# Optimization experiments

Measured on AMD Instinct MI355X. Metric: run time of the kernel, lower is better.

The kernel has to match this reference:

```python
import jax, jax.numpy as jnp
import numpy as np

B, S, HID = 2, 2048, 1024
H, D = 16, 64  # num query heads, head_dim; single shared KV head
SCALE = D ** -0.5


def setup_inputs() -> dict:
    key = jax.random.key(0)
    k1, k2, k3, k4, k5 = jax.random.split(key, 5)
    return {
        "hidden_states": jax.random.normal(k1, (B, S, HID), dtype=jnp.float32),
        "Wq": jax.random.normal(k2, (HID, HID), dtype=jnp.float32) * 0.02,
        "Wk": jax.random.normal(k3, (HID, D), dtype=jnp.float32) * 0.02,
        "Wv": jax.random.normal(k4, (HID, D), dtype=jnp.float32) * 0.02,
        "Wo": jax.random.normal(k5, (HID, HID), dtype=jnp.float32) * 0.02,
    }


def reference(hidden_states, Wq, Wk, Wv, Wo):
    b, s, _ = hidden_states.shape
    # projections: Q has H heads; K/V have a single shared head of dim D
    q = (hidden_states @ Wq).reshape(b, s, H, D)  # [B,S,H,D]
    k = hidden_states @ Wk                        # [B,S,D]
    v = hidden_states @ Wv                        # [B,S,D]
    # scores: broadcast single KV head across all query heads
    scores = jnp.einsum("bqhd,bkd->bhqk", q, k) * SCALE  # [B,H,S,S]
    attn = jax.nn.softmax(scores, axis=-1)
    out = jnp.einsum("bhqk,bkd->bqhd", attn, v).reshape(b, s, HID)
    return out @ Wo
```

## Files before the change

### kernel.cpp

```cpp
#include <hip/hip_runtime.h>
#include <math.h>

#define BATCH 2
#define SEQ   2048
#define HID   1024
#define NH    16
#define HD    64
#define MTOT  (BATCH * SEQ)

#define PST 72
#define VST 136
#define WTS 69

#define EXP_C1 0.1803368801111255f

typedef __attribute__((ext_vector_type(8))) short short8;
typedef __attribute__((ext_vector_type(4))) float floatx4;
typedef __attribute__((ext_vector_type(16))) float floatx16;
typedef __attribute__((ext_vector_type(4))) unsigned int uint4v;

#define MFMA32(a, b, c) __builtin_amdgcn_mfma_f32_32x32x16_bf16(a, b, c, 0, 0, 0)
#define MFMA16(a, b, c) __builtin_amdgcn_mfma_f32_16x16x32_bf16(a, b, c, 0, 0, 0)

static __device__ __forceinline__ floatx16 zero16() {
    floatx16 z;
    #pragma unroll
    for (int i = 0; i < 16; ++i) z[i] = 0.f;
    return z;
}

__device__ __forceinline__ unsigned short f2bf(float x) {
    unsigned u = __float_as_uint(x);
    u += 0x7FFF + ((u >> 16) & 1);
    return (unsigned short)(u >> 16);
}
__device__ __forceinline__ float bf2f(unsigned short h) {
    return __uint_as_float((unsigned)h << 16);
}

__device__ __forceinline__ void gld16(const unsigned short* g, unsigned short* l) {
    __builtin_amdgcn_global_load_lds(
        (const __attribute__((address_space(1))) unsigned int*)g,
        (__attribute__((address_space(3))) unsigned int*)l, 16, 0, 0);
}


__global__ __launch_bounds__(256)
void presplit_kernel(const float* __restrict__ Wq, const float* __restrict__ Wk,
                     const float* __restrict__ Wv, const float* __restrict__ Wo,
                     const float* __restrict__ X,
                     unsigned short* __restrict__ WqTh,
                     unsigned short* __restrict__ WkTh,
                     unsigned short* __restrict__ WvTh,
                     unsigned short* __restrict__ WoTh, unsigned short* __restrict__ WoTl,
                     unsigned short* __restrict__ Xh)
{
    __shared__ __align__(16) float Wtmp[64][WTS];
    const int tid = threadIdx.x;
    int bx = blockIdx.x;

    if (bx >= 544) {
        size_t i0 = (size_t)(bx - 544) * 4096 + tid * 16;
        float f[16];
        *(float4*)&f[0]  = *(const float4*)(X + i0 + 0);
        *(float4*)&f[4]  = *(const float4*)(X + i0 + 4);
        *(float4*)&f[8]  = *(const float4*)(X + i0 + 8);
        *(float4*)&f[12] = *(const float4*)(X + i0 + 12);
        unsigned short hh[16];
        #pragma unroll
        for (int e = 0; e < 16; ++e) hh[e] = f2bf(f[e]);
        const int m  = (bx - 544) * 4 + (tid >> 6);
        const int k0 = (tid & 63) * 16;
        const int m32 = m >> 5, mi = (m >> 4) & 1, tr = m & 15;
        #pragma unroll
        for (int c = 0; c < 2; ++c) {
            const int k = k0 + c * 8;
            const int ktx = k >> 6, ksx = (k >> 5) & 1, qd = (k >> 3) & 3;
            size_t off = (((size_t)(m32 * 16 + ktx) * 2 + ksx) * 2 + mi) * 512
                       + (qd * 16 + tr) * 8;
            *(uint4*)(Xh + off) = *(uint4*)&hh[c * 8];
        }
        return;
    }

    const float* W; unsigned short *Th, *Tl; int ldw, kt, nt;
    if (bx < 256)      { W = Wq; Th = WqTh; Tl = nullptr; ldw = HID; kt = bx >> 4; nt = bx & 15; }
    else if (bx < 272) { W = Wk; Th = WkTh; Tl = nullptr; ldw = HD;  kt = bx - 256; nt = 0; }
    else if (bx < 288) { W = Wv; Th = WvTh; Tl = nullptr; ldw = HD;  kt = bx - 272; nt = 0; }
    else               { W = Wo; Th = WoTh; Tl = WoTl;   ldw = HID; bx -= 288; kt = bx >> 4; nt = bx & 15; }
    const int k0 = kt * 64, n0 = nt * 64;

    {
        const int wk = tid >> 2, wn = (tid & 3) * 16;
        const float* wp = W + (size_t)(k0 + wk) * ldw + n0 + wn;
        float f[16];
        *(float4*)&f[0]  = *(const float4*)(wp + 0);
        *(float4*)&f[4]  = *(const float4*)(wp + 4);
        *(float4*)&f[8]  = *(const float4*)(wp + 8);
        *(float4*)&f[12] = *(const float4*)(wp + 12);
        #pragma unroll
        for (int e = 0; e < 16; ++e) Wtmp[wk][wn + e] = f[e];
    }
    __syncthreads();
    {
        const int rn = tid >> 2, rk = (tid & 3) * 16;
        float f[16];
        #pragma unroll
        for (int e = 0; e < 16; ++e) f[e] = Wtmp[rk + e][rn];
        unsigned short hh[16];
        #pragma unroll
        for (int e = 0; e < 16; ++e) hh[e] = f2bf(f[e]);
        const int sub = rn >> 4, tw = rn & 15;
        const size_t tb = ((size_t)nt * 16 + kt) * 4096;
        const int ksA = rk >> 5,       qA = (rk >> 3) & 3;
        const int ksB = (rk + 8) >> 5, qB = ((rk + 8) >> 3) & 3;
        const size_t offA = tb + (size_t)(ksA * 4 + sub) * 512 + (qA * 16 + tw) * 8;
        const size_t offB = tb + (size_t)(ksB * 4 + sub) * 512 + (qB * 16 + tw) * 8;
        *(uint4*)(Th + offA) = *(uint4*)&hh[0];
        *(uint4*)(Th + offB) = *(uint4*)&hh[8];
        if (Tl) {
            unsigned short ll[16];
            #pragma unroll
            for (int e = 0; e < 16; ++e) ll[e] = f2bf(f[e] - bf2f(hh[e]));
            *(uint4*)(Tl + offA) = *(uint4*)&ll[0];
            *(uint4*)(Tl + offB) = *(uint4*)&ll[8];
        }
    }
}

__global__ __launch_bounds__(512)
void qkv_kernel(const unsigned short* __restrict__ Xfo,
                const unsigned short* __restrict__ WqTh,
                const unsigned short* __restrict__ WkTh,
                const unsigned short* __restrict__ WvTh,
                unsigned short* __restrict__ Qh,
                unsigned short* __restrict__ Kh, unsigned short* __restrict__ Vth)
{
    __shared__ __align__(16) unsigned short Wst[2][4096];

    const int tid  = threadIdx.x;
    const int wave = tid >> 6, lane = tid & 63;
    const int t = lane & 15, quad = lane >> 4;
    const int m0 = blockIdx.x * 128;
    const int nb = blockIdx.y;

    const unsigned short *WTh; int nt;
    if (nb < 16)       { WTh = WqTh; nt = nb; }
    else if (nb == 16) { WTh = WkTh; nt = 0; }
    else               { WTh = WvTh; nt = 0; }

    floatx4 acc[4];
    #pragma unroll
    for (int sub = 0; sub < 4; ++sub) acc[sub] = (floatx4){0.f,0.f,0.f,0.f};

    const int m32 = blockIdx.x * 4 + (wave >> 1), mi = wave & 1;
    const size_t abase = ((size_t)m32 * 16) * 2048 + (size_t)mi * 512 + lane * 8;

    auto STAGE = [&](int buf, int kt) {
        const size_t tb = ((size_t)nt * 16 + kt) * 4096 + wave * 512 + lane * 8;
        gld16(WTh + tb, &Wst[buf][wave * 512]);
    };
    auto COMPUTE = [&](int buf, short8 a0, short8 a1) {
        #pragma unroll
        for (int ksq = 0; ksq < 2; ++ksq) {
            short8 am = ksq ? a1 : a0;
            #pragma unroll
            for (int sub = 0; sub < 4; ++sub) {
                short8 bh = *(const short8*)&Wst[buf][(ksq * 4 + sub) * 512 + lane * 8];
                acc[sub] = MFMA16(am, bh, acc[sub]);
            }
        }
    };

    short8 a0 = *(const short8*)(Xfo + abase);
    short8 a1 = *(const short8*)(Xfo + abase + 1024);
    STAGE(0, 0);
    __syncthreads();

    int cur = 0;
    for (int kt = 0; kt < HID / 64 - 1; ++kt) {
        STAGE(cur ^ 1, kt + 1);
        short8 n0 = *(const short8*)(Xfo + abase + (size_t)(kt + 1) * 2048);
        short8 n1 = *(const short8*)(Xfo + abase + (size_t)(kt + 1) * 2048 + 1024);

        COMPUTE(cur, a0, a1);

        __syncthreads();
        a0 = n0; a1 = n1;
        cur ^= 1;
    }
    COMPUTE(cur, a0, a1);

    #pragma unroll
    for (int sub = 0; sub < 4; ++sub)
        #pragma unroll
        for (int r = 0; r < 4; ++r) {
            int g = m0 + wave * 16 + quad * 4 + r;
            int d = sub * 16 + t;
            if (nb < 16) {
                int b = g >> 11, s = g & (SEQ - 1);
                Qh[((size_t)(b * NH + nb) * SEQ + s) * HD + d] =
                    f2bf(acc[sub][r] * EXP_C1);
            } else if (nb == 16) {
                Kh[(size_t)g * HD + d] = f2bf(acc[sub][r]);
            } else {
                int b = g >> 11, s = g & (SEQ - 1);
                Vth[(size_t)b * HD * SEQ + (size_t)d * SEQ + s] = f2bf(acc[sub][r]);
            }
        }
}

__global__ __launch_bounds__(512, 4)
void flash_kernel(const unsigned short* __restrict__ Qhg,
                  const unsigned short* __restrict__ Khg,
                  const unsigned short* __restrict__ Vthg,
                  unsigned short* __restrict__ Oh)
{
    __shared__ __align__(16) char smem[35840];
    unsigned short (*Ksh)[PST] = (unsigned short (*)[PST])smem;
    unsigned short (*Vsh)[VST] = (unsigned short (*)[VST])(smem + 18432);

    const int tid  = threadIdx.x;
    const int wave = tid >> 6, lane = tid & 63;
    const int lq = lane & 31, hi = lane >> 5;
    const int qw = wave >> 1;
    const int ks = wave & 1;
    const int klq = (lq & ~12) | ((lq & 4) << 1) | ((lq & 8) >> 1);

    const int q0 = blockIdx.x * 128;
    const int h  = blockIdx.y;
    const int b  = blockIdx.z;

    short8 qreg[4];
    {
        const unsigned short* qp =
            Qhg + ((size_t)(b * NH + h) * SEQ + q0 + qw * 32 + lq) * HD + hi * 8;
        #pragma unroll
        for (int dc = 0; dc < 4; ++dc) qreg[dc] = *(const short8*)(qp + dc * 16);
    }

    const unsigned short* Kh_b  = Khg  + (size_t)b * SEQ * HD;
    const unsigned short* Vth_b = Vthg + (size_t)b * HD * SEQ;

    const int krA = tid >> 3,          kcA = (tid & 7) * 8;
    const int krB = 64 + (tid >> 3),   kcB = kcA;
    const int vrA = tid >> 4,          vcA = (tid & 15) * 8;
    const int vrB = 32 + (tid >> 4),   vcB = vcA;

    floatx16 o0 = zero16(), o1 = zero16(), ol = zero16();
    short8 onesB;
    #pragma unroll
    for (int j = 0; j < 8; ++j) onesB[j] = (short)0x3F80;

    uint4 gk0 = *(const uint4*)(Kh_b + (size_t)krA * HD + kcA);
    uint4 gk1 = *(const uint4*)(Kh_b + (size_t)krB * HD + kcB);
    uint4 gv0 = *(const uint4*)(Vth_b + (size_t)vrA * SEQ + vcA);
    uint4 gv1 = *(const uint4*)(Vth_b + (size_t)vrB * SEQ + vcB);

    for (int kt = 0; kt < SEQ / 128; ++kt) {
        __syncthreads();
        *(uint4*)&Ksh[krA][kcA] = gk0;
        *(uint4*)&Ksh[krB][kcB] = gk1;
        *(uint4*)&Vsh[vrA][vcA] = gv0;
        *(uint4*)&Vsh[vrB][vcB] = gv1;
        if (kt + 1 < SEQ / 128) {
            gk0 = *(const uint4*)(Kh_b + (size_t)((kt + 1) * 128 + krA) * HD + kcA);
            gk1 = *(const uint4*)(Kh_b + (size_t)((kt + 1) * 128 + krB) * HD + kcB);
            gv0 = *(const uint4*)(Vth_b + (size_t)vrA * SEQ + (kt + 1) * 128 + vcA);
            gv1 = *(const uint4*)(Vth_b + (size_t)vrB * SEQ + (kt + 1) * 128 + vcB);
        }
        __syncthreads();

        #pragma unroll
        for (int c = 0; c < 2; ++c) {
            const int kb = ks * 64 + c * 32;

            floatx16 sf = zero16();
            __builtin_amdgcn_s_setprio(1);
            #pragma unroll
            for (int dc = 0; dc < 4; ++dc) {
                short8 kf = *(const short8*)&Ksh[kb + klq][dc * 16 + hi * 8];
                sf = MFMA32(kf, qreg[dc], sf);
            }
            __builtin_amdgcn_s_setprio(0);

            #pragma unroll
            for (int mm = 0; mm < 2; ++mm) {
                unsigned uu[8];
                #pragma unroll
                for (int j = 0; j < 8; ++j)
                    uu[j] = __float_as_uint(exp2f(sf[mm * 8 + j]));
                uint4v pw;
                pw.x = (uu[0] >> 16) | (uu[1] & 0xFFFF0000u);
                pw.y = (uu[2] >> 16) | (uu[3] & 0xFFFF0000u);
                pw.z = (uu[4] >> 16) | (uu[5] & 0xFFFF0000u);
                pw.w = (uu[6] >> 16) | (uu[7] & 0xFFFF0000u);
                short8 pa = __builtin_bit_cast(short8, pw);
                short8 v0 = *(const short8*)&Vsh[lq][kb + mm * 16 + hi * 8];
                short8 v1 = *(const short8*)&Vsh[32 + lq][kb + mm * 16 + hi * 8];
                __builtin_amdgcn_s_setprio(1);
                ol = MFMA32(pa, onesB, ol);
                o0 = MFMA32(pa, v0, o0);
                o1 = MFMA32(pa, v1, o1);
                __builtin_amdgcn_s_setprio(0);
            }
        }
    }

    __syncthreads();
    float* cb  = (float*)smem;
    float* cbl = (float*)(smem + 33792);
    const int cbase = (qw * 64 + lane) * 33;
    if (ks) {
        #pragma unroll
        for (int r = 0; r < 16; ++r) { cb[cbase + r] = o0[r]; cb[cbase + 16 + r] = o1[r]; }
        if (lq == 0) {
            #pragma unroll
            for (int r = 0; r < 16; ++r) cbl[(qw * 2 + hi) * 16 + r] = ol[r];
        }
    }
    __syncthreads();
    if (!ks) {
        const int m32 = b * 64 + blockIdx.x * 4 + qw;
        #pragma unroll
        for (int r = 0; r < 16; ++r) {
            int qr = (r & 3) + 8 * (r >> 2) + 4 * hi;
            float ltot = ol[r] + cbl[(qw * 2 + hi) * 16 + r];
            float inv = 1.0f / ltot;
            float a0 = o0[r] + cb[cbase + r];
            float a1 = o1[r] + cb[cbase + 16 + r];
            int mi = qr >> 4, tr = qr & 15;
            size_t base = (((size_t)(m32 * 16 + h) * 2 + 0) * 2 + mi) * 512
                        + ((lq >> 3) * 16 + tr) * 8 + (lq & 7);
            Oh[base]        = f2bf(a0 * inv);
            Oh[base + 1024] = f2bf(a1 * inv);
        }
    }
}

__global__ __launch_bounds__(512)
void out_proj_kernel(const unsigned short* __restrict__ Ofo,
                     const unsigned short* __restrict__ WoTh,
                     const unsigned short* __restrict__ WoTl,
                     float* __restrict__ out)
{
    __shared__ __align__(16) unsigned short Wst[2][2][4096];

    const int tid  = threadIdx.x;
    const int wave = tid >> 6, lane = tid & 63;
    const int t = lane & 15, quad = lane >> 4;
    const int m0 = blockIdx.x * 128;
    const int nt = blockIdx.y;

    floatx4 acc[4];
    #pragma unroll
    for (int sub = 0; sub < 4; ++sub) acc[sub] = (floatx4){0.f,0.f,0.f,0.f};

    const int m32 = blockIdx.x * 4 + (wave >> 1), mi = wave & 1;
    const size_t abase = ((size_t)m32 * 16) * 2048 + (size_t)mi * 512 + lane * 8;

    auto STAGE = [&](int buf, int kt) {
        const size_t tb = ((size_t)nt * 16 + kt) * 4096 + wave * 512 + lane * 8;
        gld16(WoTh + tb, &Wst[buf][0][wave * 512]);
        gld16(WoTl + tb, &Wst[buf][1][wave * 512]);
    };
    auto COMPUTE = [&](int buf, short8 a0, short8 a1) {
        #pragma unroll
        for (int ksq = 0; ksq < 2; ++ksq) {
            short8 am = ksq ? a1 : a0;
            #pragma unroll
            for (int sub = 0; sub < 4; ++sub) {
                short8 bh = *(const short8*)&Wst[buf][0][(ksq * 4 + sub) * 512 + lane * 8];
                short8 bl = *(const short8*)&Wst[buf][1][(ksq * 4 + sub) * 512 + lane * 8];
                acc[sub] = MFMA16(am, bh, acc[sub]);
                acc[sub] = MFMA16(am, bl, acc[sub]);
            }
        }
    };

    short8 a0 = *(const short8*)(Ofo + abase);
    short8 a1 = *(const short8*)(Ofo + abase + 1024);
    STAGE(0, 0);
    __syncthreads();

    int cur = 0;
    for (int kt = 0; kt < HID / 64 - 1; ++kt) {
        STAGE(cur ^ 1, kt + 1);
        short8 n0 = *(const short8*)(Ofo + abase + (size_t)(kt + 1) * 2048);
        short8 n1 = *(const short8*)(Ofo + abase + (size_t)(kt + 1) * 2048 + 1024);

        COMPUTE(cur, a0, a1);

        __syncthreads();
        a0 = n0; a1 = n1;
        cur ^= 1;
    }
    COMPUTE(cur, a0, a1);

    const int n0 = nt * 64;
    #pragma unroll
    for (int sub = 0; sub < 4; ++sub)
        #pragma unroll
        for (int r = 0; r < 4; ++r)
            out[(size_t)(m0 + wave * 16 + quad * 4 + r) * HID
                + n0 + sub * 16 + t] = acc[sub][r];
}

extern "C" void kernel_launch(void* const* d_in, const int* in_sizes, int n_in,
                              void* d_out, int out_size, void* d_ws, size_t ws_size,
                              hipStream_t stream)
{
    const float* X  = (const float*)d_in[0];
    const float* Wq = (const float*)d_in[1];
    const float* Wk = (const float*)d_in[2];
    const float* Wv = (const float*)d_in[3];
    const float* Wo = (const float*)d_in[4];
    float* out = (float*)d_out;

    unsigned short* Qh = (unsigned short*)d_out;
    unsigned short* Xh = Qh + (size_t)BATCH * NH * SEQ * HD;

    char* ws = (char*)d_ws;
    const size_t SZ_WQ = (size_t)HID * HID * 2;
    const size_t SZ_WK = (size_t)HD * HID * 2;
    unsigned short* WqTh = (unsigned short*)(ws);
    unsigned short* WkTh = (unsigned short*)(ws + 2*SZ_WQ);
    unsigned short* WvTh = (unsigned short*)(ws + 2*SZ_WQ + 2*SZ_WK);
    unsigned short* WoTh = (unsigned short*)(ws + 2*SZ_WQ + 4*SZ_WK);
    unsigned short* WoTl = (unsigned short*)(ws + 3*SZ_WQ + 4*SZ_WK);
    unsigned short* Kh   = (unsigned short*)(ws + 4*SZ_WQ + 4*SZ_WK);
    unsigned short* Vth  = (unsigned short*)(ws + 4*SZ_WQ + 4*SZ_WK + (size_t)MTOT*HD*2);
    unsigned short* Oh   = (unsigned short*)(ws + 4*SZ_WQ + 4*SZ_WK + (size_t)MTOT*HD*4);

    presplit_kernel<<<dim3(1568), 256, 0, stream>>>(Wq, Wk, Wv, Wo, X,
        WqTh, WkTh, WvTh, WoTh, WoTl, Xh);
    qkv_kernel<<<dim3(MTOT / 128, 18), 512, 0, stream>>>(Xh,
        WqTh, WkTh, WvTh, Qh, Kh, Vth);
    flash_kernel<<<dim3(SEQ / 128, NH, BATCH), 512, 0, stream>>>(Qh, Kh, Vth, Oh);
    out_proj_kernel<<<dim3(MTOT / 128, HID / 64), 512, 0, stream>>>(Oh, WoTh, WoTl, out);
}
```

Before: 174.4 us.

## Double-buffer K/V tiles in flash kernel with one barrier per iteration

Changes the flash attention kernel to keep two K/V tiles in dynamically sized LDS. The next tile is written into the alternate buffer while the current one is consumed, and the global prefetch for tile kt+2 is issued between the two P·V halves. Both score MFMA chains are computed up front so the two 32-key chunks get more instruction-level parallelism. This removes one of the two barriers per iteration, but doubles LDS use to about 70KB per block, which may lower occupancy from the requested 4 blocks per CU, and it holds more live registers.

```diff
diff --git a/kernel.cpp b/kernel.cpp
--- a/kernel.cpp
+++ b/kernel.cpp
@@ -11,6 +11,7 @@
 #define PST 72
 #define VST 136
 #define WTS 69
+#define FBUF 35840
 
 #define EXP_C1 0.1803368801111255f
 
@@ -216,9 +217,7 @@
                   const unsigned short* __restrict__ Vthg,
                   unsigned short* __restrict__ Oh)
 {
-    __shared__ __align__(16) char smem[35840];
-    unsigned short (*Ksh)[PST] = (unsigned short (*)[PST])smem;
-    unsigned short (*Vsh)[VST] = (unsigned short (*)[VST])(smem + 18432);
+    extern __shared__ __align__(16) char smem[];
 
     const int tid  = threadIdx.x;
     const int wave = tid >> 6, lane = tid & 63;
@@ -243,47 +242,62 @@
     const unsigned short* Vth_b = Vthg + (size_t)b * HD * SEQ;
 
     const int krA = tid >> 3,          kcA = (tid & 7) * 8;
-    const int krB = 64 + (tid >> 3),   kcB = kcA;
+    const int krB = 64 + (tid >> 3);
     const int vrA = tid >> 4,          vcA = (tid & 15) * 8;
-    const int vrB = 32 + (tid >> 4),   vcB = vcA;
+    const int vrB = 32 + (tid >> 4);
 
     floatx16 o0 = zero16(), o1 = zero16(), ol = zero16();
     short8 onesB;
     #pragma unroll
     for (int j = 0; j < 8; ++j) onesB[j] = (short)0x3F80;
 
+    const int NT = SEQ / 128;
+
     uint4 gk0 = *(const uint4*)(Kh_b + (size_t)krA * HD + kcA);
-    uint4 gk1 = *(const uint4*)(Kh_b + (size_t)krB * HD + kcB);
+    uint4 gk1 = *(const uint4*)(Kh_b + (size_t)krB * HD + kcA);
     uint4 gv0 = *(const uint4*)(Vth_b + (size_t)vrA * SEQ + vcA);
-    uint4 gv1 = *(const uint4*)(Vth_b + (size_t)vrB * SEQ + vcB);
-
-    for (int kt = 0; kt < SEQ / 128; ++kt) {
-        __syncthreads();
-        *(uint4*)&Ksh[krA][kcA] = gk0;
-        *(uint4*)&Ksh[krB][kcB] = gk1;
-        *(uint4*)&Vsh[vrA][vcA] = gv0;
-        *(uint4*)&Vsh[vrB][vcB] = gv1;
-        if (kt + 1 < SEQ / 128) {
-            gk0 = *(const uint4*)(Kh_b + (size_t)((kt + 1) * 128 + krA) * HD + kcA);
-            gk1 = *(const uint4*)(Kh_b + (size_t)((kt + 1) * 128 + krB) * HD + kcB);
-            gv0 = *(const uint4*)(Vth_b + (size_t)vrA * SEQ + (kt + 1) * 128 + vcA);
-            gv1 = *(const uint4*)(Vth_b + (size_t)vrB * SEQ + (kt + 1) * 128 + vcB);
-        }
-        __syncthreads();
-
-        #pragma unroll
-        for (int c = 0; c < 2; ++c) {
-            const int kb = ks * 64 + c * 32;
-
-            floatx16 sf = zero16();
-            __builtin_amdgcn_s_setprio(1);
-            #pragma unroll
-            for (int dc = 0; dc < 4; ++dc) {
-                short8 kf = *(const short8*)&Ksh[kb + klq][dc * 16 + hi * 8];
-                sf = MFMA32(kf, qreg[dc], sf);
-            }
-            __builtin_amdgcn_s_setprio(0);
-
+    uint4 gv1 = *(const uint4*)(Vth_b + (size_t)vrB * SEQ + vcA);
+    {
+        unsigned short (*K0)[PST] = (unsigned short (*)[PST])smem;
+        unsigned short (*V0)[VST] = (unsigned short (*)[VST])(smem + 18432);
+        *(uint4*)&K0[krA][kcA] = gk0;  *(uint4*)&K0[krB][kcA] = gk1;
+        *(uint4*)&V0[vrA][vcA] = gv0;  *(uint4*)&V0[vrB][vcA] = gv1;
+    }
+    gk0 = *(const uint4*)(Kh_b + (size_t)(128 + krA) * HD + kcA);
+    gk1 = *(const uint4*)(Kh_b + (size_t)(128 + krB) * HD + kcA);
+    gv0 = *(const uint4*)(Vth_b + (size_t)vrA * SEQ + 128 + vcA);
+    gv1 = *(const uint4*)(Vth_b + (size_t)vrB * SEQ + 128 + vcA);
+    __syncthreads();
+
+    for (int kt = 0; kt < NT; ++kt) {
+        char* base = smem + (kt & 1) * FBUF;
+        unsigned short (*Ksh)[PST] = (unsigned short (*)[PST])base;
+        unsigned short (*Vsh)[VST] = (unsigned short (*)[VST])(base + 18432);
+
+        if (kt + 1 < NT) {
+            char* nb = smem + ((kt + 1) & 1) * FBUF;
+            unsigned short (*Kw)[PST] = (unsigned short (*)[PST])nb;
+            unsigned short (*Vw)[VST] = (unsigned short (*)[VST])(nb + 18432);
+            *(uint4*)&Kw[krA][kcA] = gk0;  *(uint4*)&Kw[krB][kcA] = gk1;
+            *(uint4*)&Vw[vrA][vcA] = gv0;  *(uint4*)&Vw[vrB][vcA] = gv1;
+        }
+
+        const int kb0 = ks * 64, kb1 = ks * 64 + 32;
+        floatx16 sfA = zero16(), sfB = zero16();
+        __builtin_amdgcn_s_setprio(1);
+        #pragma unroll
+        for (int dc = 0; dc < 4; ++dc) {
+            short8 kfA = *(const short8*)&Ksh[kb0 + klq][dc * 16 + hi * 8];
+            sfA = MFMA32(kfA, qreg[dc], sfA);
+        }
+        #pragma unroll
+        for (int dc = 0; dc < 4; ++dc) {
+            short8 kfB = *(const short8*)&Ksh[kb1 + klq][dc * 16 + hi * 8];
+            sfB = MFMA32(kfB, qreg[dc], sfB);
+        }
+        __builtin_amdgcn_s_setprio(0);
+
+        auto PROCESS = [&](const floatx16& sf, int kb) {
             #pragma unroll
             for (int mm = 0; mm < 2; ++mm) {
                 unsigned uu[8];
@@ -304,10 +318,19 @@
                 o1 = MFMA32(pa, v1, o1);
                 __builtin_amdgcn_s_setprio(0);
             }
-        }
-    }
-
-    __syncthreads();
+        };
+
+        PROCESS(sfA, kb0);
+        if (kt + 2 < NT) {
+            gk0 = *(const uint4*)(Kh_b + (size_t)((kt + 2) * 128 + krA) * HD + kcA);
+            gk1 = *(const uint4*)(Kh_b + (size_t)((kt + 2) * 128 + krB) * HD + kcA);
+            gv0 = *(const uint4*)(Vth_b + (size_t)vrA * SEQ + (kt + 2) * 128 + vcA);
+            gv1 = *(const uint4*)(Vth_b + (size_t)vrB * SEQ + (kt + 2) * 128 + vcA);
+        }
+        PROCESS(sfB, kb1);
+        __syncthreads();
+    }
+
     float* cb  = (float*)smem;
     float* cbl = (float*)(smem + 33792);
     const int cbase = (qw * 64 + lane) * 33;
@@ -436,6 +459,6 @@
         WqTh, WkTh, WvTh, WoTh, WoTl, Xh);
     qkv_kernel<<<dim3(MTOT / 128, 18), 512, 0, stream>>>(Xh,
         WqTh, WkTh, WvTh, Qh, Kh, Vth);
-    flash_kernel<<<dim3(SEQ / 128, NH, BATCH), 512, 0, stream>>>(Qh, Kh, Vth, Oh);
+    flash_kernel<<<dim3(SEQ / 128, NH, BATCH), 512, 2 * FBUF, stream>>>(Qh, Kh, Vth, Oh);
     out_proj_kernel<<<dim3(MTOT / 128, HID / 64), 512, 0, stream>>>(Oh, WoTh, WoTl, out);
 }
```

Result: faster. 168.0 us (-3.7%).

## Restructure flash attention with tiled swizzled KV layout and async LDS double-buffering

Applied to the files above, without the earlier changes.

The QKV projection now writes Q, K and V in 128-row tiles with XOR swizzling, so the flash kernel can copy whole tiles into LDS with global_load_lds into double buffers and avoid register staging. The flash kernel moves to 1024 threads with a 4-way key split per query group, keeps Q in LDS, and replaces the ones-matrix MFMA row-sum with a scalar partial sum of the bf16-truncated exponentials. The partial results are reduced across four waves through LDS in sequential rounds. This costs 80KB of dynamic LDS per block, which limits occupancy, and adds extra reduction syncs.

```diff
diff --git a/kernel.cpp b/kernel.cpp
--- a/kernel.cpp
+++ b/kernel.cpp
@@ -8,9 +8,10 @@
 #define HD    64
 #define MTOT  (BATCH * SEQ)
 
-#define PST 72
-#define VST 136
 #define WTS 69
+
+#define FSTG 32768
+#define FQOF 65536
 
 #define EXP_C1 0.1803368801111255f
 
@@ -42,6 +43,10 @@
     __builtin_amdgcn_global_load_lds(
         (const __attribute__((address_space(1))) unsigned int*)g,
         (__attribute__((address_space(3))) unsigned int*)l, 16, 0, 0);
+}
+
+__device__ __forceinline__ unsigned packtr(unsigned hi, unsigned lo) {
+    return __builtin_amdgcn_perm(hi, lo, 0x07060302u);
 }
 
 
@@ -133,8 +138,8 @@
                 const unsigned short* __restrict__ WqTh,
                 const unsigned short* __restrict__ WkTh,
                 const unsigned short* __restrict__ WvTh,
-                unsigned short* __restrict__ Qh,
-                unsigned short* __restrict__ Kh, unsigned short* __restrict__ Vth)
+                unsigned short* __restrict__ Qhf,
+                unsigned short* __restrict__ Khf, unsigned short* __restrict__ Vthf)
 {
     __shared__ __align__(16) unsigned short Wst[2][4096];
 
@@ -197,143 +202,139 @@
         for (int r = 0; r < 4; ++r) {
             int g = m0 + wave * 16 + quad * 4 + r;
             int d = sub * 16 + t;
+            int b = g >> 11, sfull = g & (SEQ - 1);
+            int tt = sfull >> 7, sl = sfull & 127;
+            int xor8 = (sl & 7) << 3;
             if (nb < 16) {
-                int b = g >> 11, s = g & (SEQ - 1);
-                Qh[((size_t)(b * NH + nb) * SEQ + s) * HD + d] =
+                Qhf[(((size_t)(b * NH + nb) * 16 + tt) * 8192) + sl * 64 + (d ^ xor8)] =
                     f2bf(acc[sub][r] * EXP_C1);
             } else if (nb == 16) {
-                Kh[(size_t)g * HD + d] = f2bf(acc[sub][r]);
+                Khf[((size_t)b * 16 + tt) * 8192 + sl * 64 + (d ^ xor8)] =
+                    f2bf(acc[sub][r]);
             } else {
-                int b = g >> 11, s = g & (SEQ - 1);
-                Vth[(size_t)b * HD * SEQ + (size_t)d * SEQ + s] = f2bf(acc[sub][r]);
+                Vthf[((size_t)b * 16 + tt) * 8192 + d * 128 + (sl ^ ((d & 7) << 3))] =
+                    f2bf(acc[sub][r]);
             }
         }
 }
 
-__global__ __launch_bounds__(512, 4)
-void flash_kernel(const unsigned short* __restrict__ Qhg,
-                  const unsigned short* __restrict__ Khg,
-                  const unsigned short* __restrict__ Vthg,
+__global__ __launch_bounds__(1024, 8)
+void flash_kernel(const unsigned short* __restrict__ Qhf,
+                  const unsigned short* __restrict__ Khf,
+                  const unsigned short* __restrict__ Vthf,
                   unsigned short* __restrict__ Oh)
 {
-    __shared__ __align__(16) char smem[35840];
-    unsigned short (*Ksh)[PST] = (unsigned short (*)[PST])smem;
-    unsigned short (*Vsh)[VST] = (unsigned short (*)[VST])(smem + 18432);
+    extern __shared__ __align__(16) char smem[];
 
     const int tid  = threadIdx.x;
     const int wave = tid >> 6, lane = tid & 63;
     const int lq = lane & 31, hi = lane >> 5;
-    const int qw = wave >> 1;
-    const int ks = wave & 1;
+    const int qg = wave >> 2;
+    const int kq = wave & 3;
     const int klq = (lq & ~12) | ((lq & 4) << 1) | ((lq & 8) >> 1);
 
-    const int q0 = blockIdx.x * 128;
     const int h  = blockIdx.y;
     const int b  = blockIdx.z;
 
-    short8 qreg[4];
+    const unsigned short* Qt = Qhf + (((size_t)(b * NH + h) * 16 + blockIdx.x) * 8192);
+    const unsigned short* Kb = Khf + ((size_t)b * 16) * 8192;
+    const unsigned short* Vb = Vthf + ((size_t)b * 16) * 8192;
+
+    unsigned short* Qlds = (unsigned short*)(smem + FQOF);
+
+    floatx16 o0 = zero16(), o1 = zero16();
+    float l_part = 0.f;
+
+    const int NT = SEQ / 128;
+
+    gld16(Qt + tid * 8, Qlds + tid * 8);
     {
-        const unsigned short* qp =
-            Qhg + ((size_t)(b * NH + h) * SEQ + q0 + qw * 32 + lq) * HD + hi * 8;
-        #pragma unroll
-        for (int dc = 0; dc < 4; ++dc) qreg[dc] = *(const short8*)(qp + dc * 16);
-    }
-
-    const unsigned short* Kh_b  = Khg  + (size_t)b * SEQ * HD;
-    const unsigned short* Vth_b = Vthg + (size_t)b * HD * SEQ;
-
-    const int krA = tid >> 3,          kcA = (tid & 7) * 8;
-    const int krB = 64 + (tid >> 3),   kcB = kcA;
-    const int vrA = tid >> 4,          vcA = (tid & 15) * 8;
-    const int vrB = 32 + (tid >> 4),   vcB = vcA;
-
-    floatx16 o0 = zero16(), o1 = zero16(), ol = zero16();
-    short8 onesB;
-    #pragma unroll
-    for (int j = 0; j < 8; ++j) onesB[j] = (short)0x3F80;
-
-    uint4 gk0 = *(const uint4*)(Kh_b + (size_t)krA * HD + kcA);
-    uint4 gk1 = *(const uint4*)(Kh_b + (size_t)krB * HD + kcB);
-    uint4 gv0 = *(const uint4*)(Vth_b + (size_t)vrA * SEQ + vcA);
-    uint4 gv1 = *(const uint4*)(Vth_b + (size_t)vrB * SEQ + vcB);
-
-    for (int kt = 0; kt < SEQ / 128; ++kt) {
+        unsigned short* K0 = (unsigned short*)(smem);
+        unsigned short* V0 = (unsigned short*)(smem + 16384);
+        gld16(Kb + tid * 8, K0 + tid * 8);
+        gld16(Vb + tid * 8, V0 + tid * 8);
+    }
+    __syncthreads();
+
+    const int kb = kq * 32;
+    const int qrow = qg * 32 + lq;
+    const int qxor = (lq & 7) << 3;
+    const int vxor = (lq & 7) << 3;
+
+    for (int kt = 0; kt < NT; ++kt) {
+        unsigned short* Kl = (unsigned short*)(smem + (kt & 1) * FSTG);
+        unsigned short* Vl = (unsigned short*)(smem + (kt & 1) * FSTG + 16384);
+
+        if (kt + 1 < NT) {
+            unsigned short* Kn = (unsigned short*)(smem + ((kt + 1) & 1) * FSTG);
+            unsigned short* Vn = (unsigned short*)(smem + ((kt + 1) & 1) * FSTG + 16384);
+            gld16(Kb + (size_t)(kt + 1) * 8192 + tid * 8, Kn + tid * 8);
+            gld16(Vb + (size_t)(kt + 1) * 8192 + tid * 8, Vn + tid * 8);
+        }
+
+        floatx16 sf = zero16();
+        __builtin_amdgcn_s_setprio(1);
+        #pragma unroll
+        for (int dc = 0; dc < 4; ++dc) {
+            const int col = dc * 16 + hi * 8;
+            short8 kf = *(const short8*)&Kl[(kb + klq) * 64 + (col ^ ((klq & 7) << 3))];
+            short8 qf = *(const short8*)&Qlds[qrow * 64 + (col ^ qxor)];
+            sf = MFMA32(kf, qf, sf);
+        }
+        __builtin_amdgcn_s_setprio(0);
+
+        #pragma unroll
+        for (int mm = 0; mm < 2; ++mm) {
+            uint4v pw;
+            #pragma unroll
+            for (int wj = 0; wj < 4; ++wj) {
+                unsigned e0 = __float_as_uint(exp2f(sf[mm * 8 + wj * 2]));
+                unsigned e1 = __float_as_uint(exp2f(sf[mm * 8 + wj * 2 + 1]));
+                l_part += __uint_as_float(e0 & 0xFFFF0000u)
+                        + __uint_as_float(e1 & 0xFFFF0000u);
+                pw[wj] = packtr(e1, e0);
+            }
+            short8 pa = __builtin_bit_cast(short8, pw);
+            const int scol = kb + mm * 16 + hi * 8;
+            short8 v0 = *(const short8*)&Vl[lq * 128 + (scol ^ vxor)];
+            short8 v1 = *(const short8*)&Vl[(32 + lq) * 128 + (scol ^ vxor)];
+            __builtin_amdgcn_s_setprio(1);
+            o0 = MFMA32(pa, v0, o0);
+            o1 = MFMA32(pa, v1, o1);
+            __builtin_amdgcn_s_setprio(0);
+        }
         __syncthreads();
-        *(uint4*)&Ksh[krA][kcA] = gk0;
-        *(uint4*)&Ksh[krB][kcB] = gk1;
-        *(uint4*)&Vsh[vrA][vcA] = gv0;
-        *(uint4*)&Vsh[vrB][vcB] = gv1;
-        if (kt + 1 < SEQ / 128) {
-            gk0 = *(const uint4*)(Kh_b + (size_t)((kt + 1) * 128 + krA) * HD + kcA);
-            gk1 = *(const uint4*)(Kh_b + (size_t)((kt + 1) * 128 + krB) * HD + kcB);
-            gv0 = *(const uint4*)(Vth_b + (size_t)vrA * SEQ + (kt + 1) * 128 + vcA);
-            gv1 = *(const uint4*)(Vth_b + (size_t)vrB * SEQ + (kt + 1) * 128 + vcB);
+    }
+
+    float l_wave = l_part + __shfl_xor(l_part, 32);
+    float* cb = (float*)smem;
+    const int cbase = (qg * 64 + lane) * 33;
+    #pragma unroll
+    for (int rr = 1; rr < 4; ++rr) {
+        if (kq == rr) {
+            #pragma unroll
+            for (int r = 0; r < 16; ++r) { cb[cbase + r] = o0[r]; cb[cbase + 16 + r] = o1[r]; }
+            cb[cbase + 32] = l_wave;
         }
         __syncthreads();
-
-        #pragma unroll
-        for (int c = 0; c < 2; ++c) {
-            const int kb = ks * 64 + c * 32;
-
-            floatx16 sf = zero16();
-            __builtin_amdgcn_s_setprio(1);
-            #pragma unroll
-            for (int dc = 0; dc < 4; ++dc) {
-                short8 kf = *(const short8*)&Ksh[kb + klq][dc * 16 + hi * 8];
-                sf = MFMA32(kf, qreg[dc], sf);
-            }
-            __builtin_amdgcn_s_setprio(0);
-
-            #pragma unroll
-            for (int mm = 0; mm < 2; ++mm) {
-                unsigned uu[8];
-                #pragma unroll
-                for (int j = 0; j < 8; ++j)
-                    uu[j] = __float_as_uint(exp2f(sf[mm * 8 + j]));
-                uint4v pw;
-                pw.x = (uu[0] >> 16) | (uu[1] & 0xFFFF0000u);
-                pw.y = (uu[2] >> 16) | (uu[3] & 0xFFFF0000u);
-                pw.z = (uu[4] >> 16) | (uu[5] & 0xFFFF0000u);
-                pw.w = (uu[6] >> 16) | (uu[7] & 0xFFFF0000u);
-                short8 pa = __builtin_bit_cast(short8, pw);
-                short8 v0 = *(const short8*)&Vsh[lq][kb + mm * 16 + hi * 8];
-                short8 v1 = *(const short8*)&Vsh[32 + lq][kb + mm * 16 + hi * 8];
-                __builtin_amdgcn_s_setprio(1);
-                ol = MFMA32(pa, onesB, ol);
-                o0 = MFMA32(pa, v0, o0);
-                o1 = MFMA32(pa, v1, o1);
-                __builtin_amdgcn_s_setprio(0);
-            }
-        }
-    }
-
-    __syncthreads();
-    float* cb  = (float*)smem;
-    float* cbl = (float*)(smem + 33792);
-    const int cbase = (qw * 64 + lane) * 33;
-    if (ks) {
-        #pragma unroll
-        for (int r = 0; r < 16; ++r) { cb[cbase + r] = o0[r]; cb[cbase + 16 + r] = o1[r]; }
-        if (lq == 0) {
-            #pragma unroll
-            for (int r = 0; r < 16; ++r) cbl[(qw * 2 + hi) * 16 + r] = ol[r];
-        }
-    }
-    __syncthreads();
-    if (!ks) {
-        const int m32 = b * 64 + blockIdx.x * 4 + qw;
+        if (kq == 0) {
+            #pragma unroll
+            for (int r = 0; r < 16; ++r) { o0[r] += cb[cbase + r]; o1[r] += cb[cbase + 16 + r]; }
+            l_wave += cb[cbase + 32];
+        }
+        __syncthreads();
+    }
+    if (kq == 0) {
+        const int m32 = b * 64 + blockIdx.x * 4 + qg;
         #pragma unroll
         for (int r = 0; r < 16; ++r) {
             int qr = (r & 3) + 8 * (r >> 2) + 4 * hi;
-            float ltot = ol[r] + cbl[(qw * 2 + hi) * 16 + r];
-            float inv = 1.0f / ltot;
-            float a0 = o0[r] + cb[cbase + r];
-            float a1 = o1[r] + cb[cbase + 16 + r];
+            float inv = 1.0f / __shfl(l_wave, qr);
             int mi = qr >> 4, tr = qr & 15;
             size_t base = (((size_t)(m32 * 16 + h) * 2 + 0) * 2 + mi) * 512
                         + ((lq >> 3) * 16 + tr) * 8 + (lq & 7);
-            Oh[base]        = f2bf(a0 * inv);
-            Oh[base + 1024] = f2bf(a1 * inv);
+            Oh[base]        = f2bf(o0[r] * inv);
+            Oh[base + 1024] = f2bf(o1[r] * inv);
         }
     }
 }
@@ -417,8 +418,8 @@
     const float* Wo = (const float*)d_in[4];
     float* out = (float*)d_out;
 
-    unsigned short* Qh = (unsigned short*)d_out;
-    unsigned short* Xh = Qh + (size_t)BATCH * NH * SEQ * HD;
+    unsigned short* Qhf = (unsigned short*)d_out;
+    unsigned short* Xh  = Qhf + (size_t)BATCH * NH * SEQ * HD;
 
     char* ws = (char*)d_ws;
     const size_t SZ_WQ = (size_t)HID * HID * 2;
@@ -428,14 +429,15 @@
     unsigned short* WvTh = (unsigned short*)(ws + 2*SZ_WQ + 2*SZ_WK);
     unsigned short* WoTh = (unsigned short*)(ws + 2*SZ_WQ + 4*SZ_WK);
     unsigned short* WoTl = (unsigned short*)(ws + 3*SZ_WQ + 4*SZ_WK);
-    unsigned short* Kh   = (unsigned short*)(ws + 4*SZ_WQ + 4*SZ_WK);
-    unsigned short* Vth  = (unsigned short*)(ws + 4*SZ_WQ + 4*SZ_WK + (size_t)MTOT*HD*2);
+    unsigned short* Khf  = (unsigned short*)(ws + 4*SZ_WQ + 4*SZ_WK);
+    unsigned short* Vthf = (unsigned short*)(ws + 4*SZ_WQ + 4*SZ_WK + (size_t)MTOT*HD*2);
     unsigned short* Oh   = (unsigned short*)(ws + 4*SZ_WQ + 4*SZ_WK + (size_t)MTOT*HD*4);
 
     presplit_kernel<<<dim3(1568), 256, 0, stream>>>(Wq, Wk, Wv, Wo, X,
         WqTh, WkTh, WvTh, WoTh, WoTl, Xh);
     qkv_kernel<<<dim3(MTOT / 128, 18), 512, 0, stream>>>(Xh,
-        WqTh, WkTh, WvTh, Qh, Kh, Vth);
-    flash_kernel<<<dim3(SEQ / 128, NH, BATCH), 512, 0, stream>>>(Qh, Kh, Vth, Oh);
+        WqTh, WkTh, WvTh, Qhf, Khf, Vthf);
+    flash_kernel<<<dim3(SEQ / 128, NH, BATCH), 1024, 2 * FSTG + 16384, stream>>>(
+        Qhf, Khf, Vthf, Oh);
     out_proj_kernel<<<dim3(MTOT / 128, HID / 64), 512, 0, stream>>>(Oh, WoTh, WoTl, out);
 }
```

Result: slower. 384.7 us (+120.6%).
